# Kernel optimization log

Measured on AMD Instinct MI355X. Metric: run time of the kernel, lower is better.

## Reference

```python
import jax, jax.numpy as jnp
import numpy as np

N = 100_000
E = 1_600_000
D_IN = 128
D_HID = 128
D_OUT = 16
K = 3  # PyG TAGConv default number of hops


def setup_inputs() -> dict:
    key = jax.random.key(0)
    ks = jax.random.split(key, 5)
    x = jax.random.normal(ks[0], (N, D_IN), dtype=jnp.float32)
    edge_index = jax.random.randint(ks[1], (2, E), 0, N, dtype=jnp.int32)
    # TAGConv has (K+1) bias-free linear layers + one shared bias per conv
    W1 = jax.random.normal(ks[2], (K + 1, D_IN, D_HID), dtype=jnp.float32) * 0.05
    b1 = jnp.zeros((D_HID,), dtype=jnp.float32)
    W2 = jax.random.normal(ks[3], (K + 1, D_HID, D_OUT), dtype=jnp.float32) * 0.05
    b2 = jnp.zeros((D_OUT,), dtype=jnp.float32)
    return {"x": x, "edge_index": edge_index, "W1": W1, "b1": b1, "W2": W2, "b2": b2}


def _tag_conv(x, src, dst, norm, W, b):
    # out = sum_{k=0..K} (A_norm^k x) @ W[k] + b
    out = x @ W[0]
    h = x
    for k in range(1, W.shape[0]):
        msg = h[src] * norm[:, None]                      # [E, d] gather
        h = jax.ops.segment_sum(msg, dst, num_segments=x.shape[0])  # scatter-add
        out = out + h @ W[k]
    return out + b


def reference(x, edge_index, W1, b1, W2, b2):
    src, dst = edge_index[0], edge_index[1]
    # gcn_norm without self-loops: deg over target nodes
    deg = jax.ops.segment_sum(jnp.ones((src.shape[0],), x.dtype), dst, num_segments=x.shape[0])
    dis = jnp.where(deg > 0, jax.lax.rsqrt(jnp.maximum(deg, 1.0)), 0.0).astype(x.dtype)
    norm = dis[src] * dis[dst]
    h = jax.nn.relu(_tag_conv(x, src, dst, norm, W1, b1))
    return _tag_conv(h, src, dst, norm, W2, b2)
```

## Files before the change

### kernel.cpp

```cpp
#include <hip/hip_runtime.h>

#define DF 128

typedef __attribute__((ext_vector_type(8))) short bf16x8;
typedef __attribute__((ext_vector_type(4))) float f32x4;

__device__ __forceinline__ ushort f2bf(float f) {
  uint u = __float_as_uint(f);
  u += 0x7fff + ((u >> 16) & 1);
  return (ushort)(u >> 16);
}
__device__ __forceinline__ float bfl(uint v) { return __uint_as_float(v << 16); }
__device__ __forceinline__ float bfh(uint v) { return __uint_as_float(v & 0xffff0000u); }
__device__ __forceinline__ float b2f(ushort s) { return __uint_as_float(((uint)s) << 16); }

__global__ __launch_bounds__(256) void prepw_k(const float* __restrict__ W1, const float* __restrict__ W2,
                                               ushort* __restrict__ W1f, ushort* __restrict__ W2f,
                                               ushort* __restrict__ Z3s, ushort* __restrict__ T,
                                               ushort* __restrict__ GBs3, ushort* __restrict__ F0,
                                               ushort* __restrict__ F1, int n) {
  int b = blockIdx.x, tid = threadIdx.x;
  if (b == 256) {
    if (tid < 128) {
      Z3s[(size_t)n * 128 + tid] = 0;
      T[(size_t)n * 128 + tid] = 0;
    }
    if (tid < 16) {
      GBs3[(size_t)n * 16 + tid] = 0;
      F0[(size_t)n * 16 + tid] = 0;
      F1[(size_t)n * 16 + tid] = 0;
    }
    return;
  }
  int t = b * 256 + tid;
  {
    int k = t >> 14, rem = t & 16383;
    int frag = rem >> 3, j = rem & 7;
    int nt = frag >> 8, ks = (frag >> 6) & 3, lane = frag & 63;
    int nn = nt * 16 + (lane & 15);
    int kk = ks * 32 + (lane >> 4) * 8 + j;
    W1f[t] = f2bf(W1[k * 16384 + kk * 128 + nn]);
  }
  if (t < 8192) {
    int frag = t >> 3, j = t & 7;
    int nt = frag >> 8, ks = (frag >> 6) & 3, lane = frag & 63;
    int kk = ks * 32 + (lane >> 4) * 8 + j;
    W2f[t] = f2bf(W2[nt * 2048 + kk * 16 + (lane & 15)]);
  }
}

__global__ __launch_bounds__(256) void k1_k(const float* __restrict__ x, const ushort* __restrict__ W1f,
                                            ushort* __restrict__ Z3, ushort* __restrict__ Z2,
                                            ushort* __restrict__ Z1, ushort* __restrict__ Z0,
                                            const int* __restrict__ dst, int e,
                                            int* __restrict__ deg_s, int* __restrict__ rank,
                                            int n, int GZ) {
  int b = blockIdx.x, tid = threadIdx.x;
  if (b >= GZ) {
    int i = (b - GZ) * 256 + tid;
    if (i < e) {
      int shard = (i >> 8) & 7;
      rank[i] = atomicAdd(&deg_s[(size_t)shard * n + dst[i]], 1);
    }
    return;
  }
  int wid = tid >> 6, lane = tid & 63;
  int l15 = lane & 15, kgrp = lane >> 4;
  int m0 = b * 128 + wid * 32 + l15;
  int m1 = m0 + 16;
  int mc0 = m0 < n ? m0 : n - 1;
  int mc1 = m1 < n ? m1 : n - 1;
  bf16x8 xf0[4], xf1[4];
#pragma unroll
  for (int ks = 0; ks < 4; ks++) {
    float4 a0 = *reinterpret_cast<const float4*>(x + (size_t)mc0 * 128 + ks * 32 + kgrp * 8);
    float4 a1 = *reinterpret_cast<const float4*>(x + (size_t)mc0 * 128 + ks * 32 + kgrp * 8 + 4);
    float4 b0 = *reinterpret_cast<const float4*>(x + (size_t)mc1 * 128 + ks * 32 + kgrp * 8);
    float4 b1v = *reinterpret_cast<const float4*>(x + (size_t)mc1 * 128 + ks * 32 + kgrp * 8 + 4);
    bf16x8 u, w;
    u[0] = (short)f2bf(a0.x); u[1] = (short)f2bf(a0.y); u[2] = (short)f2bf(a0.z); u[3] = (short)f2bf(a0.w);
    u[4] = (short)f2bf(a1.x); u[5] = (short)f2bf(a1.y); u[6] = (short)f2bf(a1.z); u[7] = (short)f2bf(a1.w);
    w[0] = (short)f2bf(b0.x); w[1] = (short)f2bf(b0.y); w[2] = (short)f2bf(b0.z); w[3] = (short)f2bf(b0.w);
    w[4] = (short)f2bf(b1v.x); w[5] = (short)f2bf(b1v.y); w[6] = (short)f2bf(b1v.z); w[7] = (short)f2bf(b1v.w);
    xf0[ks] = u; xf1[ks] = w;
  }
#pragma unroll
  for (int kk = 0; kk < 4; kk++) {
    const int k = 3 - kk;
    const ushort* Wk = W1f + (size_t)k * 16384;
    ushort* Out = (k == 3) ? Z3 : (k == 2) ? Z2 : (k == 1) ? Z1 : Z0;
#pragma unroll
    for (int nt = 0; nt < 8; nt++) {
      f32x4 acc0 = {0.f, 0.f, 0.f, 0.f}, acc1 = {0.f, 0.f, 0.f, 0.f};
#pragma unroll
      for (int ks = 0; ks < 4; ks++) {
        bf16x8 wf = *reinterpret_cast<const bf16x8*>(Wk + (size_t)((nt * 4 + ks) * 64 + lane) * 8);
        acc0 = __builtin_amdgcn_mfma_f32_16x16x32_bf16(wf, xf0[ks], acc0, 0, 0, 0);
        acc1 = __builtin_amdgcn_mfma_f32_16x16x32_bf16(wf, xf1[ks], acc1, 0, 0, 0);
      }
      int ncol = nt * 16 + kgrp * 4;
      if (m0 < n) {
        ushort4 st; st.x = f2bf(acc0[0]); st.y = f2bf(acc0[1]);
        st.z = f2bf(acc0[2]); st.w = f2bf(acc0[3]);
        *reinterpret_cast<ushort4*>(Out + (size_t)m0 * 128 + ncol) = st;
      }
      if (m1 < n) {
        ushort4 st; st.x = f2bf(acc1[0]); st.y = f2bf(acc1[1]);
        st.z = f2bf(acc1[2]); st.w = f2bf(acc1[3]);
        *reinterpret_cast<ushort4*>(Out + (size_t)m1 * 128 + ncol) = st;
      }
    }
  }
}

__global__ __launch_bounds__(256) void rs1_k(const int* __restrict__ deg_s, int n,
                                             int* __restrict__ deg, int* __restrict__ P,
                                             float* __restrict__ dis, int* __restrict__ partials) {
  __shared__ int sm[256];
  int tid = threadIdx.x;
  int base = blockIdx.x * 1024;
  int s = 0;
#pragma unroll
  for (int j = 0; j < 4; j++) {
    int idx = base + tid * 4 + j;
    if (idx < n) {
      int run = 0;
#pragma unroll
      for (int sh = 0; sh < 8; sh++) {
        int v = deg_s[(size_t)sh * n + idx];
        P[(size_t)sh * n + idx] = run;
        run += v;
      }
      deg[idx] = run;
      dis[idx] = run > 0 ? rsqrtf((float)run) : 0.f;
      s += run;
    }
  }
  sm[tid] = s; __syncthreads();
  for (int off = 128; off > 0; off >>= 1) {
    if (tid < off) sm[tid] += sm[tid + off];
    __syncthreads();
  }
  if (tid == 0) partials[blockIdx.x] = sm[0];
}

__global__ void scan2_k(int* partials, int nb) {
  if (threadIdx.x == 0 && blockIdx.x == 0) {
    int run = 0;
    for (int i = 0; i < nb; i++) { int v = partials[i]; partials[i] = run; run += v; }
  }
}

__global__ __launch_bounds__(256) void scan3_k(const int* __restrict__ deg, int n, int e,
                                               const int* __restrict__ partials,
                                               int* __restrict__ rowptr,
                                               const int* __restrict__ P, int* __restrict__ base8) {
  __shared__ int sm[256];
  int base = blockIdx.x * 1024;
  int loc[4]; int s = 0;
#pragma unroll
  for (int j = 0; j < 4; j++) {
    int idx = base + threadIdx.x * 4 + j;
    int v = (idx < n) ? deg[idx] : 0;
    loc[j] = s; s += v;
  }
  sm[threadIdx.x] = s; __syncthreads();
  int tsum = s;
  for (int off = 1; off < 256; off <<= 1) {
    int v = (threadIdx.x >= (unsigned)off) ? sm[threadIdx.x - off] : 0;
    __syncthreads();
    sm[threadIdx.x] += v;
    __syncthreads();
  }
  int excl = sm[threadIdx.x] - tsum + partials[blockIdx.x];
#pragma unroll
  for (int j = 0; j < 4; j++) {
    int idx = base + threadIdx.x * 4 + j;
    if (idx < n) {
      int rp = excl + loc[j];
      rowptr[idx] = rp;
#pragma unroll
      for (int sh = 0; sh < 8; sh++)
        base8[(size_t)sh * n + idx] = rp + P[(size_t)sh * n + idx];
    }
  }
  if (blockIdx.x == 0 && threadIdx.x == 0) rowptr[n] = e;
}

__global__ __launch_bounds__(256) void k2_k(const int* __restrict__ src, const int* __restrict__ dst, int e,
                                            const int* __restrict__ rank, const int* __restrict__ base8,
                                            int* __restrict__ colb,
                                            ushort* __restrict__ Z3, const float* __restrict__ dis,
                                            int n, int gE) {
  int b = blockIdx.x, tid = threadIdx.x;
  if (b < gE) {
    int i = b * 256 + tid;
    if (i < e) {
      int d = dst[i];
      int shard = (i >> 8) & 7;
      int p = base8[(size_t)shard * n + d] + rank[i];
      colb[p] = src[i];
    }
  } else {
    int u = (b - gE) * 256 + tid;
    int i = u >> 4, seg = u & 15;
    if (i < n) {
      float d = dis[i];
      ushort* p = Z3 + (size_t)i * 128 + seg * 8;
      uint4 v = *reinterpret_cast<const uint4*>(p);
      uint4 o;
      o.x = (uint)f2bf(d * bfl(v.x)) | ((uint)f2bf(d * bfh(v.x)) << 16);
      o.y = (uint)f2bf(d * bfl(v.y)) | ((uint)f2bf(d * bfh(v.y)) << 16);
      o.z = (uint)f2bf(d * bfl(v.z)) | ((uint)f2bf(d * bfh(v.z)) << 16);
      o.w = (uint)f2bf(d * bfl(v.w)) | ((uint)f2bf(d * bfh(v.w)) << 16);
      *reinterpret_cast<uint4*>(p) = o;
    }
  }
}

__global__ __launch_bounds__(256) void hop_k(const ushort* __restrict__ hin, const ushort* __restrict__ zk,
                                             const float* __restrict__ b1, ushort* __restrict__ hout,
                                             const int* __restrict__ rowptr, const int* __restrict__ colb,
                                             const float* __restrict__ dis, int n, int gHop, int last) {
  int colhalf = blockIdx.x >= gHop ? 1 : 0;
  int nb = blockIdx.x - colhalf * gHop;
  int node = nb * 16 + (threadIdx.x >> 4);
  int gl = threadIdx.x & 15;
  if (node >= n) return;
  int cbase = colhalf * 64 + gl * 4;
  int e0 = rowptr[node], e1 = rowptr[node + 1];
  float a0 = 0.f, a1 = 0.f, a2 = 0.f, a3 = 0.f;
  for (int ee = e0; ee < e1; ee += 16) {
    int c[16];
#pragma unroll
    for (int j = 0; j < 16; j++) {
      int idx = ee + j;
      c[j] = idx < e1 ? colb[idx] : n;
    }
    uint2 v[16];
#pragma unroll
    for (int j = 0; j < 16; j++)
      v[j] = *reinterpret_cast<const uint2*>(hin + (size_t)c[j] * 128 + cbase);
#pragma unroll
    for (int j = 0; j < 16; j++) {
      a0 += bfl(v[j].x); a1 += bfh(v[j].x);
      a2 += bfl(v[j].y); a3 += bfh(v[j].y);
    }
  }
  float d = dis[node];
  uint2 zr = *reinterpret_cast<const uint2*>(zk + (size_t)node * 128 + cbase);
  float t0 = fmaf(d, a0, bfl(zr.x)), t1 = fmaf(d, a1, bfh(zr.x));
  float t2 = fmaf(d, a2, bfl(zr.y)), t3 = fmaf(d, a3, bfh(zr.y));
  uint2 st;
  if (last) {
    float4 bv = *reinterpret_cast<const float4*>(b1 + cbase);
    t0 = fmaxf(t0 + bv.x, 0.f); t1 = fmaxf(t1 + bv.y, 0.f);
    t2 = fmaxf(t2 + bv.z, 0.f); t3 = fmaxf(t3 + bv.w, 0.f);
    st.x = (uint)f2bf(t0) | ((uint)f2bf(t1) << 16);
    st.y = (uint)f2bf(t2) | ((uint)f2bf(t3) << 16);
  } else {
    st.x = (uint)f2bf(d * t0) | ((uint)f2bf(d * t1) << 16);
    st.y = (uint)f2bf(d * t2) | ((uint)f2bf(d * t3) << 16);
  }
  *reinterpret_cast<uint2*>(hout + (size_t)node * 128 + cbase) = st;
}

__global__ __launch_bounds__(256) void gemm_last_k(const ushort* __restrict__ h1, const ushort* __restrict__ W2f,
                                                   const float* __restrict__ dis,
                                                   ushort* __restrict__ GB, ushort* __restrict__ GBs3, int n) {
  int wid = threadIdx.x >> 6, lane = threadIdx.x & 63;
  int kgrp = lane >> 4;
  int m = blockIdx.x * 64 + wid * 16 + (lane & 15);
  int mc = m < n ? m : n - 1;
  float dm = dis[mc];
  bf16x8 xf[4];
#pragma unroll
  for (int ks = 0; ks < 4; ks++)
    xf[ks] = *reinterpret_cast<const bf16x8*>(h1 + (size_t)mc * 128 + ks * 32 + kgrp * 8);
#pragma unroll
  for (int nt = 0; nt < 4; nt++) {
    f32x4 acc = {0.f, 0.f, 0.f, 0.f};
#pragma unroll
    for (int ks = 0; ks < 4; ks++) {
      bf16x8 wf = *reinterpret_cast<const bf16x8*>(W2f + (size_t)((nt * 4 + ks) * 64 + lane) * 8);
      acc = __builtin_amdgcn_mfma_f32_16x16x32_bf16(wf, xf[ks], acc, 0, 0, 0);
    }
    if (m < n) {
      int ncol = nt * 16 + kgrp * 4;
      ushort4 st; st.x = f2bf(acc[0]); st.y = f2bf(acc[1]); st.z = f2bf(acc[2]); st.w = f2bf(acc[3]);
      *reinterpret_cast<ushort4*>(GB + (size_t)m * 64 + ncol) = st;
      if (nt == 3) {
        ushort4 ss; ss.x = f2bf(dm * acc[0]); ss.y = f2bf(dm * acc[1]);
        ss.z = f2bf(dm * acc[2]); ss.w = f2bf(dm * acc[3]);
        *reinterpret_cast<ushort4*>(GBs3 + (size_t)m * 16 + kgrp * 4) = ss;
      }
    }
  }
}

__global__ __launch_bounds__(256) void spmm16_k(const ushort* __restrict__ in,
                                                const ushort* __restrict__ addraw, int addstride,
                                                const float* __restrict__ b2,
                                                float* __restrict__ outf, ushort* __restrict__ outb,
                                                const int* __restrict__ rowptr, const int* __restrict__ colb,
                                                const float* __restrict__ dis, int n) {
  int t = blockIdx.x * 256 + threadIdx.x;
  int node = t >> 3, cp = t & 7;
  if (node >= n) return;
  int e0 = rowptr[node], e1 = rowptr[node + 1];
  float a0 = 0.f, a1 = 0.f;
  for (int ee = e0; ee < e1; ee += 8) {
    int c[8];
#pragma unroll
    for (int j = 0; j < 8; j++) {
      int idx = ee + j;
      c[j] = idx < e1 ? colb[idx] : n;
    }
    uint v[8];
#pragma unroll
    for (int j = 0; j < 8; j++)
      v[j] = *reinterpret_cast<const uint*>(in + (size_t)c[j] * 16 + cp * 2);
#pragma unroll
    for (int j = 0; j < 8; j++) { a0 += bfl(v[j]); a1 += bfh(v[j]); }
  }
  float d = dis[node];
  uint av = *reinterpret_cast<const uint*>(addraw + (size_t)node * addstride + cp * 2);
  float t0 = fmaf(d, a0, b2f((ushort)(av & 0xffff)));
  float t1 = fmaf(d, a1, b2f((ushort)(av >> 16)));
  if (outf) {
    float2 st; st.x = t0 + b2[cp * 2]; st.y = t1 + b2[cp * 2 + 1];
    *reinterpret_cast<float2*>(outf + (size_t)node * 16 + cp * 2) = st;
  } else {
    uint pk = (uint)f2bf(d * t0) | ((uint)f2bf(d * t1) << 16);
    *reinterpret_cast<uint*>(outb + (size_t)node * 16 + cp * 2) = pk;
  }
}

extern "C" void kernel_launch(void* const* d_in, const int* in_sizes, int n_in,
                              void* d_out, int out_size, void* d_ws, size_t ws_size,
                              hipStream_t stream) {
  const float* x  = (const float*)d_in[0];
  const int*   ei = (const int*)d_in[1];
  const float* W1 = (const float*)d_in[2];
  const float* b1 = (const float*)d_in[3];
  const float* W2 = (const float*)d_in[4];
  const float* b2 = (const float*)d_in[5];
  float* out = (float*)d_out;

  const int n = in_sizes[0] / DF;
  const int e = in_sizes[1] / 2;
  const int* srcp = ei;
  const int* dstp = ei + e;

  char* ws = (char*)d_ws;
  size_t off = 0;
  auto alloc = [&](size_t bytes) -> void* {
    void* p = ws + off;
    off += (bytes + 255) & ~(size_t)255;
    return p;
  };
  ushort* Z3s  = (ushort*)alloc((size_t)(n + 1) * 128 * 2);
  ushort* T    = (ushort*)alloc((size_t)(n + 1) * 128 * 2);
  ushort* Z2   = (ushort*)alloc((size_t)n * 128 * 2);
  ushort* Z1   = (ushort*)alloc((size_t)n * 128 * 2);
  ushort* Z0   = (ushort*)alloc((size_t)n * 128 * 2);
  int*   deg_s = (int*)alloc((size_t)8 * n * 4);
  int*   P     = (int*)alloc((size_t)8 * n * 4);
  int*   deg   = (int*)alloc((size_t)n * 4);
  float* dis   = (float*)alloc((size_t)n * 4);
  int*   rowptr= (int*)alloc((size_t)(n + 1) * 4);
  int*   rank  = (int*)alloc((size_t)e * 4);
  int*   partials = (int*)alloc(1024 * 4);
  int*   colb  = (int*)alloc((size_t)e * 4);
  ushort* W1f  = (ushort*)alloc(4 * 128 * 128 * 2);
  ushort* W2f  = (ushort*)alloc(64 * 128 * 2);
  ushort* GBs3 = (ushort*)alloc((size_t)(n + 1) * 16 * 2);
  ushort* F0   = (ushort*)alloc((size_t)(n + 1) * 16 * 2);
  ushort* F1   = (ushort*)alloc((size_t)(n + 1) * 16 * 2);
  ushort* Up = Z3s;
  ushort* h1 = T;
  ushort* GB = Z2;
  int* base8 = deg_s;

  hipMemsetAsync(deg_s, 0, (size_t)8 * n * 4, stream);

  int gE = (e + 255) / 256;
  int nb = (n + 1023) / 1024;
  int GZ = (n + 127) / 128;

  prepw_k<<<257, 256, 0, stream>>>(W1, W2, W1f, W2f, Z3s, T, GBs3, F0, F1, n);
  k1_k<<<GZ + gE, 256, 0, stream>>>(x, W1f, Z3s, Z2, Z1, Z0, dstp, e, deg_s, rank, n, GZ);
  rs1_k<<<nb, 256, 0, stream>>>(deg_s, n, deg, P, dis, partials);
  scan2_k<<<1, 64, 0, stream>>>(partials, nb);
  scan3_k<<<nb, 256, 0, stream>>>(deg, n, e, partials, rowptr, P, base8);
  int gScale = (n * 16 + 255) / 256;
  k2_k<<<gE + gScale, 256, 0, stream>>>(srcp, dstp, e, rank, base8, colb, Z3s, dis, n, gE);

  int gHop = (n + 15) / 16;
  int gGemm = (n + 63) / 64;
  int gS16 = (n * 8 + 255) / 256;

  hop_k<<<2 * gHop, 256, 0, stream>>>(Z3s, Z2, nullptr, T, rowptr, colb, dis, n, gHop, 0);
  hop_k<<<2 * gHop, 256, 0, stream>>>(T, Z1, nullptr, Up, rowptr, colb, dis, n, gHop, 0);
  hop_k<<<2 * gHop, 256, 0, stream>>>(Up, Z0, b1, h1, rowptr, colb, dis, n, gHop, 1);
  gemm_last_k<<<gGemm, 256, 0, stream>>>(h1, W2f, dis, GB, GBs3, n);

  spmm16_k<<<gS16, 256, 0, stream>>>(GBs3, GB + 32, 64, nullptr, nullptr, F0, rowptr, colb, dis, n);
  spmm16_k<<<gS16, 256, 0, stream>>>(F0,   GB + 16, 64, nullptr, nullptr, F1, rowptr, colb, dis, n);
  spmm16_k<<<gS16, 256, 0, stream>>>(F1,   GB + 0,  64, b2, out, nullptr, rowptr, colb, dis, n);
}
```

Measured before the change: 402.6 us.

## Fold Z3 dis-scaling into first hop gather and drop serial partial scan

Removes the separate pass that rescaled Z3 by dis in place, applying a per-source dis weight inside the first hop's gather instead. The single-thread scan2 kernel is replaced by each scan3 block reducing the preceding partials itself. The launch order changes: the histogram runs alone first, and the GEMM is then fused with the CSR column fill. The first hop pays an extra random dis load per edge in exchange for skipping a full read-write pass over Z3 and one serial kernel, but the GEMM no longer overlaps with the atomic histogram.

New measurement: 438.3 us. +8.9%, slower.

```diff
diff --git a/kernel.cpp b/kernel.cpp
--- a/kernel.cpp
+++ b/kernel.cpp
@@ -16,13 +16,13 @@
 
 __global__ __launch_bounds__(256) void prepw_k(const float* __restrict__ W1, const float* __restrict__ W2,
                                                ushort* __restrict__ W1f, ushort* __restrict__ W2f,
-                                               ushort* __restrict__ Z3s, ushort* __restrict__ T,
+                                               ushort* __restrict__ Z3r, ushort* __restrict__ T,
                                                ushort* __restrict__ GBs3, ushort* __restrict__ F0,
                                                ushort* __restrict__ F1, int n) {
   int b = blockIdx.x, tid = threadIdx.x;
   if (b == 256) {
     if (tid < 128) {
-      Z3s[(size_t)n * 128 + tid] = 0;
+      Z3r[(size_t)n * 128 + tid] = 0;
       T[(size_t)n * 128 + tid] = 0;
     }
     if (tid < 16) {
@@ -49,18 +49,107 @@
   }
 }
 
-__global__ __launch_bounds__(256) void k1_k(const float* __restrict__ x, const ushort* __restrict__ W1f,
+__global__ __launch_bounds__(256) void hist_k(const int* __restrict__ dst, int e,
+                                              int* __restrict__ deg_s, int* __restrict__ rank, int n) {
+  int i = blockIdx.x * 256 + threadIdx.x;
+  if (i < e) {
+    int shard = (i >> 8) & 7;
+    rank[i] = atomicAdd(&deg_s[(size_t)shard * n + dst[i]], 1);
+  }
+}
+
+__global__ __launch_bounds__(256) void rs1_k(const int* __restrict__ deg_s, int n,
+                                             int* __restrict__ deg, int* __restrict__ P,
+                                             float* __restrict__ dis, int* __restrict__ partials) {
+  __shared__ int sm[256];
+  int tid = threadIdx.x;
+  if (blockIdx.x == 0 && tid == 0) dis[n] = 0.f;
+  int base = blockIdx.x * 1024;
+  int s = 0;
+#pragma unroll
+  for (int j = 0; j < 4; j++) {
+    int idx = base + tid * 4 + j;
+    if (idx < n) {
+      int run = 0;
+#pragma unroll
+      for (int sh = 0; sh < 8; sh++) {
+        int v = deg_s[(size_t)sh * n + idx];
+        P[(size_t)sh * n + idx] = run;
+        run += v;
+      }
+      deg[idx] = run;
+      dis[idx] = run > 0 ? rsqrtf((float)run) : 0.f;
+      s += run;
+    }
+  }
+  sm[tid] = s; __syncthreads();
+  for (int off = 128; off > 0; off >>= 1) {
+    if (tid < off) sm[tid] += sm[tid + off];
+    __syncthreads();
+  }
+  if (tid == 0) partials[blockIdx.x] = sm[0];
+}
+
+__global__ __launch_bounds__(256) void scan3_k(const int* __restrict__ deg, int n, int e,
+                                               const int* __restrict__ partials,
+                                               int* __restrict__ rowptr,
+                                               const int* __restrict__ P, int* __restrict__ base8) {
+  __shared__ int sm[256];
+  __shared__ int pp[256];
+  int tid = threadIdx.x;
+  int pre = 0;
+  for (int i = tid; i < blockIdx.x; i += 256) pre += partials[i];
+  pp[tid] = pre; __syncthreads();
+  for (int off = 128; off > 0; off >>= 1) {
+    if (tid < off) pp[tid] += pp[tid + off];
+    __syncthreads();
+  }
+  int blockbase = pp[0];
+  int base = blockIdx.x * 1024;
+  int loc[4]; int s = 0;
+#pragma unroll
+  for (int j = 0; j < 4; j++) {
+    int idx = base + tid * 4 + j;
+    int v = (idx < n) ? deg[idx] : 0;
+    loc[j] = s; s += v;
+  }
+  sm[tid] = s; __syncthreads();
+  int tsum = s;
+  for (int off = 1; off < 256; off <<= 1) {
+    int v = (tid >= (unsigned)off) ? sm[tid - off] : 0;
+    __syncthreads();
+    sm[tid] += v;
+    __syncthreads();
+  }
+  int excl = sm[tid] - tsum + blockbase;
+#pragma unroll
+  for (int j = 0; j < 4; j++) {
+    int idx = base + tid * 4 + j;
+    if (idx < n) {
+      int rp = excl + loc[j];
+      rowptr[idx] = rp;
+#pragma unroll
+      for (int sh = 0; sh < 8; sh++)
+        base8[(size_t)sh * n + idx] = rp + P[(size_t)sh * n + idx];
+    }
+  }
+  if (blockIdx.x == 0 && tid == 0) rowptr[n] = e;
+}
+
+__global__ __launch_bounds__(256) void k2_k(const float* __restrict__ x, const ushort* __restrict__ W1f,
                                             ushort* __restrict__ Z3, ushort* __restrict__ Z2,
                                             ushort* __restrict__ Z1, ushort* __restrict__ Z0,
-                                            const int* __restrict__ dst, int e,
-                                            int* __restrict__ deg_s, int* __restrict__ rank,
-                                            int n, int GZ) {
+                                            const int* __restrict__ src, const int* __restrict__ dst, int e,
+                                            const int* __restrict__ rank, const int* __restrict__ base8,
+                                            int* __restrict__ colb, int n, int GZ) {
   int b = blockIdx.x, tid = threadIdx.x;
   if (b >= GZ) {
     int i = (b - GZ) * 256 + tid;
     if (i < e) {
+      int d = dst[i];
       int shard = (i >> 8) & 7;
-      rank[i] = atomicAdd(&deg_s[(size_t)shard * n + dst[i]], 1);
+      int p = base8[(size_t)shard * n + d] + rank[i];
+      colb[p] = src[i];
     }
     return;
   }
@@ -113,115 +202,11 @@
   }
 }
 
-__global__ __launch_bounds__(256) void rs1_k(const int* __restrict__ deg_s, int n,
-                                             int* __restrict__ deg, int* __restrict__ P,
-                                             float* __restrict__ dis, int* __restrict__ partials) {
-  __shared__ int sm[256];
-  int tid = threadIdx.x;
-  int base = blockIdx.x * 1024;
-  int s = 0;
-#pragma unroll
-  for (int j = 0; j < 4; j++) {
-    int idx = base + tid * 4 + j;
-    if (idx < n) {
-      int run = 0;
-#pragma unroll
-      for (int sh = 0; sh < 8; sh++) {
-        int v = deg_s[(size_t)sh * n + idx];
-        P[(size_t)sh * n + idx] = run;
-        run += v;
-      }
-      deg[idx] = run;
-      dis[idx] = run > 0 ? rsqrtf((float)run) : 0.f;
-      s += run;
-    }
-  }
-  sm[tid] = s; __syncthreads();
-  for (int off = 128; off > 0; off >>= 1) {
-    if (tid < off) sm[tid] += sm[tid + off];
-    __syncthreads();
-  }
-  if (tid == 0) partials[blockIdx.x] = sm[0];
-}
-
-__global__ void scan2_k(int* partials, int nb) {
-  if (threadIdx.x == 0 && blockIdx.x == 0) {
-    int run = 0;
-    for (int i = 0; i < nb; i++) { int v = partials[i]; partials[i] = run; run += v; }
-  }
-}
-
-__global__ __launch_bounds__(256) void scan3_k(const int* __restrict__ deg, int n, int e,
-                                               const int* __restrict__ partials,
-                                               int* __restrict__ rowptr,
-                                               const int* __restrict__ P, int* __restrict__ base8) {
-  __shared__ int sm[256];
-  int base = blockIdx.x * 1024;
-  int loc[4]; int s = 0;
-#pragma unroll
-  for (int j = 0; j < 4; j++) {
-    int idx = base + threadIdx.x * 4 + j;
-    int v = (idx < n) ? deg[idx] : 0;
-    loc[j] = s; s += v;
-  }
-  sm[threadIdx.x] = s; __syncthreads();
-  int tsum = s;
-  for (int off = 1; off < 256; off <<= 1) {
-    int v = (threadIdx.x >= (unsigned)off) ? sm[threadIdx.x - off] : 0;
-    __syncthreads();
-    sm[threadIdx.x] += v;
-    __syncthreads();
-  }
-  int excl = sm[threadIdx.x] - tsum + partials[blockIdx.x];
-#pragma unroll
-  for (int j = 0; j < 4; j++) {
-    int idx = base + threadIdx.x * 4 + j;
-    if (idx < n) {
-      int rp = excl + loc[j];
-      rowptr[idx] = rp;
-#pragma unroll
-      for (int sh = 0; sh < 8; sh++)
-        base8[(size_t)sh * n + idx] = rp + P[(size_t)sh * n + idx];
-    }
-  }
-  if (blockIdx.x == 0 && threadIdx.x == 0) rowptr[n] = e;
-}
-
-__global__ __launch_bounds__(256) void k2_k(const int* __restrict__ src, const int* __restrict__ dst, int e,
-                                            const int* __restrict__ rank, const int* __restrict__ base8,
-                                            int* __restrict__ colb,
-                                            ushort* __restrict__ Z3, const float* __restrict__ dis,
-                                            int n, int gE) {
-  int b = blockIdx.x, tid = threadIdx.x;
-  if (b < gE) {
-    int i = b * 256 + tid;
-    if (i < e) {
-      int d = dst[i];
-      int shard = (i >> 8) & 7;
-      int p = base8[(size_t)shard * n + d] + rank[i];
-      colb[p] = src[i];
-    }
-  } else {
-    int u = (b - gE) * 256 + tid;
-    int i = u >> 4, seg = u & 15;
-    if (i < n) {
-      float d = dis[i];
-      ushort* p = Z3 + (size_t)i * 128 + seg * 8;
-      uint4 v = *reinterpret_cast<const uint4*>(p);
-      uint4 o;
-      o.x = (uint)f2bf(d * bfl(v.x)) | ((uint)f2bf(d * bfh(v.x)) << 16);
-      o.y = (uint)f2bf(d * bfl(v.y)) | ((uint)f2bf(d * bfh(v.y)) << 16);
-      o.z = (uint)f2bf(d * bfl(v.z)) | ((uint)f2bf(d * bfh(v.z)) << 16);
-      o.w = (uint)f2bf(d * bfl(v.w)) | ((uint)f2bf(d * bfh(v.w)) << 16);
-      *reinterpret_cast<uint4*>(p) = o;
-    }
-  }
-}
-
 __global__ __launch_bounds__(256) void hop_k(const ushort* __restrict__ hin, const ushort* __restrict__ zk,
                                              const float* __restrict__ b1, ushort* __restrict__ hout,
                                              const int* __restrict__ rowptr, const int* __restrict__ colb,
-                                             const float* __restrict__ dis, int n, int gHop, int last) {
+                                             const float* __restrict__ dis, const float* __restrict__ dscale,
+                                             int n, int gHop, int last) {
   int colhalf = blockIdx.x >= gHop ? 1 : 0;
   int nb = blockIdx.x - colhalf * gHop;
   int node = nb * 16 + (threadIdx.x >> 4);
@@ -241,10 +226,21 @@
 #pragma unroll
     for (int j = 0; j < 16; j++)
       v[j] = *reinterpret_cast<const uint2*>(hin + (size_t)c[j] * 128 + cbase);
-#pragma unroll
-    for (int j = 0; j < 16; j++) {
-      a0 += bfl(v[j].x); a1 += bfh(v[j].x);
-      a2 += bfl(v[j].y); a3 += bfh(v[j].y);
+    if (dscale) {
+      float w[16];
+#pragma unroll
+      for (int j = 0; j < 16; j++) w[j] = dscale[c[j]];
+#pragma unroll
+      for (int j = 0; j < 16; j++) {
+        a0 = fmaf(w[j], bfl(v[j].x), a0); a1 = fmaf(w[j], bfh(v[j].x), a1);
+        a2 = fmaf(w[j], bfl(v[j].y), a2); a3 = fmaf(w[j], bfh(v[j].y), a3);
+      }
+    } else {
+#pragma unroll
+      for (int j = 0; j < 16; j++) {
+        a0 += bfl(v[j].x); a1 += bfh(v[j].x);
+        a2 += bfl(v[j].y); a3 += bfh(v[j].y);
+      }
     }
   }
   float d = dis[node];
@@ -359,7 +355,7 @@
     off += (bytes + 255) & ~(size_t)255;
     return p;
   };
-  ushort* Z3s  = (ushort*)alloc((size_t)(n + 1) * 128 * 2);
+  ushort* Z3r  = (ushort*)alloc((size_t)(n + 1) * 128 * 2);
   ushort* T    = (ushort*)alloc((size_t)(n + 1) * 128 * 2);
   ushort* Z2   = (ushort*)alloc((size_t)n * 128 * 2);
   ushort* Z1   = (ushort*)alloc((size_t)n * 128 * 2);
@@ -367,7 +363,7 @@
   int*   deg_s = (int*)alloc((size_t)8 * n * 4);
   int*   P     = (int*)alloc((size_t)8 * n * 4);
   int*   deg   = (int*)alloc((size_t)n * 4);
-  float* dis   = (float*)alloc((size_t)n * 4);
+  float* dis   = (float*)alloc((size_t)(n + 1) * 4);
   int*   rowptr= (int*)alloc((size_t)(n + 1) * 4);
   int*   rank  = (int*)alloc((size_t)e * 4);
   int*   partials = (int*)alloc(1024 * 4);
@@ -377,7 +373,7 @@
   ushort* GBs3 = (ushort*)alloc((size_t)(n + 1) * 16 * 2);
   ushort* F0   = (ushort*)alloc((size_t)(n + 1) * 16 * 2);
   ushort* F1   = (ushort*)alloc((size_t)(n + 1) * 16 * 2);
-  ushort* Up = Z3s;
+  ushort* Up = Z3r;
   ushort* h1 = T;
   ushort* GB = Z2;
   int* base8 = deg_s;
@@ -388,21 +384,19 @@
   int nb = (n + 1023) / 1024;
   int GZ = (n + 127) / 128;
 
-  prepw_k<<<257, 256, 0, stream>>>(W1, W2, W1f, W2f, Z3s, T, GBs3, F0, F1, n);
-  k1_k<<<GZ + gE, 256, 0, stream>>>(x, W1f, Z3s, Z2, Z1, Z0, dstp, e, deg_s, rank, n, GZ);
+  prepw_k<<<257, 256, 0, stream>>>(W1, W2, W1f, W2f, Z3r, T, GBs3, F0, F1, n);
+  hist_k<<<gE, 256, 0, stream>>>(dstp, e, deg_s, rank, n);
   rs1_k<<<nb, 256, 0, stream>>>(deg_s, n, deg, P, dis, partials);
-  scan2_k<<<1, 64, 0, stream>>>(partials, nb);
   scan3_k<<<nb, 256, 0, stream>>>(deg, n, e, partials, rowptr, P, base8);
-  int gScale = (n * 16 + 255) / 256;
-  k2_k<<<gE + gScale, 256, 0, stream>>>(srcp, dstp, e, rank, base8, colb, Z3s, dis, n, gE);
+  k2_k<<<GZ + gE, 256, 0, stream>>>(x, W1f, Z3r, Z2, Z1, Z0, srcp, dstp, e, rank, base8, colb, n, GZ);
 
   int gHop = (n + 15) / 16;
   int gGemm = (n + 63) / 64;
   int gS16 = (n * 8 + 255) / 256;
 
-  hop_k<<<2 * gHop, 256, 0, stream>>>(Z3s, Z2, nullptr, T, rowptr, colb, dis, n, gHop, 0);
-  hop_k<<<2 * gHop, 256, 0, stream>>>(T, Z1, nullptr, Up, rowptr, colb, dis, n, gHop, 0);
-  hop_k<<<2 * gHop, 256, 0, stream>>>(Up, Z0, b1, h1, rowptr, colb, dis, n, gHop, 1);
+  hop_k<<<2 * gHop, 256, 0, stream>>>(Z3r, Z2, nullptr, T, rowptr, colb, dis, dis, n, gHop, 0);
+  hop_k<<<2 * gHop, 256, 0, stream>>>(T, Z1, nullptr, Up, rowptr, colb, dis, nullptr, n, gHop, 0);
+  hop_k<<<2 * gHop, 256, 0, stream>>>(Up, Z0, b1, h1, rowptr, colb, dis, nullptr, n, gHop, 1);
   gemm_last_k<<<gGemm, 256, 0, stream>>>(h1, W2f, dis, GB, GBs3, n);
 
   spmm16_k<<<gS16, 256, 0, stream>>>(GBs3, GB + 32, 64, nullptr, nullptr, F0, rowptr, colb, dis, n);
```
